# Performance work log

Measured on AMD Instinct MI355X. Metric: run time of the kernel, lower is better.

The kernel has to match this reference:

```python
import jax, jax.numpy as jnp
import numpy as np

L, N, K = 512, 64, 38      # seq_len, batch, input feature size
E, H = 1024, 1024          # embed_size, hidden_size
NUM_LAYERS = 3
C = 38                     # num_classes


def setup_inputs() -> dict:
    key = jax.random.key(0)
    ks = jax.random.split(key, 9)
    s_e = 1.0 / np.sqrt(K)
    s_h = 1.0 / np.sqrt(H)
    return {
        "inputs": jax.random.normal(ks[0], (L, N, K), jnp.float32),
        "emb_W": jax.random.uniform(ks[1], (E, K), jnp.float32, -s_e, s_e),
        "emb_b": jnp.zeros((E,), jnp.float32),
        # GRU weights, PyTorch layout: gates ordered (r, z, n) along 3H axis
        "w_ih": jax.random.uniform(ks[2], (NUM_LAYERS, 3 * H, E), jnp.float32, -s_h, s_h),
        "w_hh": jax.random.uniform(ks[3], (NUM_LAYERS, 3 * H, H), jnp.float32, -s_h, s_h),
        "b_ih": jax.random.uniform(ks[4], (NUM_LAYERS, 3 * H), jnp.float32, -s_h, s_h),
        "b_hh": jax.random.uniform(ks[5], (NUM_LAYERS, 3 * H), jnp.float32, -s_h, s_h),
        "out_W": jax.random.uniform(ks[6], (C, H), jnp.float32, -s_h, s_h),
        "out_b": jnp.zeros((C,), jnp.float32),
    }


def _gru_layer(x, w_ih, w_hh, b_ih, b_hh):
    # x: (L, N, in_dim) -> outputs (L, N, H), final hidden (N, H)
    # Precompute all input projections as one big GEMM: (L, N, 3H)
    xg = jnp.einsum('lni,gi->lng', x, w_ih) + b_ih
    h0 = jnp.zeros((x.shape[1], H), x.dtype)

    def step(h, xg_t):
        hg = h @ w_hh.T + b_hh                      # (N, 3H)
        xr, xz, xn = jnp.split(xg_t, 3, axis=-1)
        hr, hz, hn = jnp.split(hg, 3, axis=-1)
        r = jax.nn.sigmoid(xr + hr)
        z = jax.nn.sigmoid(xz + hz)
        n = jnp.tanh(xn + r * hn)
        h_new = (1.0 - z) * n + z * h
        return h_new, h_new

    h_last, outs = jax.lax.scan(step, h0, xg)
    return outs, h_last


def reference(inputs, emb_W, emb_b, w_ih, w_hh, b_ih, b_hh, out_W, out_b):
    # embedding: Linear(K -> E), applied per timestep
    x = jnp.einsum('lnk,ek->lne', inputs, emb_W) + emb_b  # (L, N, E)
    for l in range(NUM_LAYERS):  # fixed structural loop over layers
        x, _ = _gru_layer(x, w_ih[l], w_hh[l], b_ih[l], b_hh[l])
    # output projection: Linear(H -> C)
    logit = jnp.einsum('lnh,ch->lnc', x, out_W) + out_b    # (L, N, C)
    return logit
```

## Files before the change

kernel.cpp:

```cpp
#include <hip/hip_runtime.h>
#include <hip/hip_fp16.h>
#include <stdint.h>
#include <stddef.h>

typedef _Float16 f16;
typedef _Float16 f16x8 __attribute__((ext_vector_type(8)));
typedef float f32x4 __attribute__((ext_vector_type(4)));

#define SEQL 512
#define NBATCH 64
#define KIN 38
#define KPAD 64
#define EMB 1024
#define HID 1024
#define G3 3072
#define MALL (SEQL*NBATCH)
#define NCLS 38
#define WPAD 1032
#define FS 32


__global__ void k_cvt(const float* __restrict__ s, f16* __restrict__ d, long n) {
  long i = (long)blockIdx.x * blockDim.x + threadIdx.x;
  long stride = (long)gridDim.x * blockDim.x;
  for (; i < n; i += stride) d[i] = (f16)s[i];
}

__global__ void k_zero(int* __restrict__ p, int n) {
  int i = blockIdx.x * 256 + threadIdx.x;
  if (i < n) p[i] = 0;
}

__global__ void k_outw_pad(const float* __restrict__ s, f16* __restrict__ d) {
  int i = blockIdx.x * 256 + threadIdx.x;
  if (i >= 128 * 1024) return;
  int r = i >> 10, c = i & 1023;
  d[i] = (r < NCLS) ? (f16)s[r * 1024 + c] : (f16)0.f;
}

__global__ void k_cvt_in(const float* __restrict__ s, f16* __restrict__ d) {
  int i = blockIdx.x * 256 + threadIdx.x;
  if (i >= MALL * KPAD) return;
  int m = i >> 6, k = i & 63;
  d[i] = (k < KIN) ? (f16)s[m * KIN + k] : (f16)0.f;
}

__global__ void k_prep_w0(const float* __restrict__ wih0, const float* __restrict__ embW,
                          f16* __restrict__ w0) {
  int i = blockIdx.x * 256 + threadIdx.x;
  if (i >= G3 * KPAD) return;
  int g = i >> 6, k = i & 63;
  float sacc = 0.f;
  if (k < KIN) {
    for (int e = 0; e < EMB; ++e) sacc += wih0[g * EMB + e] * embW[e * KIN + k];
  }
  w0[i] = (f16)sacc;
}

__global__ void k_prep_b0(const float* __restrict__ wih0, const float* __restrict__ embB,
                          const float* __restrict__ bih0, float* __restrict__ b0) {
  int g = blockIdx.x * 256 + threadIdx.x;
  if (g >= G3) return;
  float sacc = bih0[g];
  for (int e = 0; e < EMB; ++e) sacc += wih0[g * EMB + e] * embB[e];
  b0[g] = sacc;
}


__global__ __launch_bounds__(256) void k_gemm(
    const f16* __restrict__ A, const f16* __restrict__ B,
    const float* __restrict__ bias,
    f16* __restrict__ C16, float* __restrict__ C32,
    int K, int nvalid, int ldc) {
  __shared__ f16 As[128][40];
  __shared__ f16 Bs[128][40];
  const int tid = threadIdx.x;
  const long brow = (long)blockIdx.x * 128;
  const long bcol = (long)blockIdx.y * 128;
  const int w = tid >> 6, lane = tid & 63;
  const int lr = lane & 15, kg = lane >> 4;
  const int wr = w >> 1, wc = w & 1;

  f32x4 acc[4][4] = {};

  for (int kk = 0; kk < K; kk += 32) {
    __syncthreads();
#pragma unroll
    for (int p = 0; p < 2; ++p) {
      int idx = p * 256 + tid;
      int row = idx >> 2, seg = idx & 3;
      *(float4*)(&As[row][seg * 8]) = *(const float4*)(&A[(brow + row) * K + kk + seg * 8]);
      *(float4*)(&Bs[row][seg * 8]) = *(const float4*)(&B[(bcol + row) * K + kk + seg * 8]);
    }
    __syncthreads();
    f16x8 af[4], bf[4];
#pragma unroll
    for (int i = 0; i < 4; ++i) af[i] = *(const f16x8*)(&As[wr * 64 + i * 16 + lr][kg * 8]);
#pragma unroll
    for (int j = 0; j < 4; ++j) bf[j] = *(const f16x8*)(&Bs[wc * 64 + j * 16 + lr][kg * 8]);
#pragma unroll
    for (int i = 0; i < 4; ++i)
#pragma unroll
      for (int j = 0; j < 4; ++j)
        acc[i][j] = __builtin_amdgcn_mfma_f32_16x16x32_f16(af[i], bf[j], acc[i][j], 0, 0, 0);
  }

#pragma unroll
  for (int j = 0; j < 4; ++j) {
    int col = (int)bcol + wc * 64 + j * 16 + lr;
    float bv = (col < nvalid) ? bias[col] : 0.f;
#pragma unroll
    for (int i = 0; i < 4; ++i) {
#pragma unroll
      for (int r = 0; r < 4; ++r) {
        long row = brow + wr * 64 + i * 16 + kg * 4 + r;
        float v = acc[i][j][r] + bv;
        if (C16) C16[row * ldc + col] = (f16)v;
        else if (col < nvalid) C32[row * ldc + col] = v;
      }
    }
  }
}


__global__ __launch_bounds__(256) void k_rnn(
    f16* __restrict__ xseq,
    f16* __restrict__ hbuf,
    const f16* __restrict__ xg,
    const f16* __restrict__ whhl,
    const float* __restrict__ bhhl,
    int t0, int T, int base,
    int* __restrict__ flags) {
  __shared__ f16 wlds[48 * WPAD];
  const int g = blockIdx.x, j0 = g * 16, tid = threadIdx.x;
  const int w = tid >> 6, lane = tid & 63, lr = lane & 15, kg = lane >> 4;

  for (int idx = tid; idx < 48 * 128; idx += 256) {
    int row = idx >> 7, seg = idx & 127;
    int gt = row >> 4, r = row & 15;
    *(f16x8*)&wlds[row * WPAD + seg * 8] =
        *(const f16x8*)&whhl[(size_t)((gt << 10) + j0 + r) * HID + seg * 8];
  }
  __syncthreads();

  const int j = j0 + lr;
  const float br = bhhl[j], bz = bhhl[1024 + j], bn = bhhl[2048 + j];
  const f16* wr_ = &wlds[(0 * 16 + lr) * WPAD];
  const f16* wz_ = &wlds[(1 * 16 + lr) * WPAD];
  const f16* wn_ = &wlds[(2 * 16 + lr) * WPAD];

  f16 pxr[4], pxz[4], pxn[4];
#pragma unroll
  for (int r = 0; r < 4; ++r) {
    int m = 16 * w + kg * 4 + r;
    pxr[r] = xg[m * G3 + j];
    pxz[r] = xg[m * G3 + 1024 + j];
    pxn[r] = xg[m * G3 + 2048 + j];
  }

  for (int tt = 0; tt < T; ++tt) {
    const int t = t0 + tt;
    f32x4 ar = {}, az = {}, an = {};
    float hp4[4] = {0.f, 0.f, 0.f, 0.f};
    if (t > 0) {
      const int target = base + t;
      int v;
      do {
        v = __hip_atomic_load(&flags[lane * FS], __ATOMIC_ACQUIRE, __HIP_MEMORY_SCOPE_AGENT);
      } while (!__all(v >= target));
      const f16* hb = hbuf + (((t & 1) ^ 1) ? (size_t)(NBATCH * HID) : 0);
      const f16* hbp = hb + g * 1024;
#pragma unroll
      for (int r = 0; r < 4; ++r)
        hp4[r] = (float)hbp[(16 * w + kg * 4 + r) * 16 + lr];
      const f16* hbase = hb + (16 * w + lr) * 16 + (kg & 1) * 8 + (kg >> 1) * 1024;
#pragma unroll 8
      for (int kc = 0; kc < 32; ++kc) {
        f16x8 a = *(const f16x8*)(hbase + kc * 2048);
        int ko = kc * 32 + kg * 8;
        ar = __builtin_amdgcn_mfma_f32_16x16x32_f16(a, *(const f16x8*)(wr_ + ko), ar, 0, 0, 0);
        az = __builtin_amdgcn_mfma_f32_16x16x32_f16(a, *(const f16x8*)(wz_ + ko), az, 0, 0, 0);
        an = __builtin_amdgcn_mfma_f32_16x16x32_f16(a, *(const f16x8*)(wn_ + ko), an, 0, 0, 0);
      }
    }
    f16* hbn = hbuf + ((t & 1) ? (size_t)(NBATCH * HID) : 0) + g * 1024;
    f16* xrow = xseq + (size_t)t * (NBATCH * HID);
#pragma unroll
    for (int r = 0; r < 4; ++r) {
      int m = 16 * w + kg * 4 + r;
      float xr = (float)pxr[r], xz = (float)pxz[r], xn = (float)pxn[r];
      float rr = 1.f / (1.f + __expf(-(xr + ar[r] + br)));
      float zz = 1.f / (1.f + __expf(-(xz + az[r] + bz)));
      float pre = xn + rr * (an[r] + bn);
      float nn = 2.f / (1.f + __expf(-2.f * pre)) - 1.f;
      float hv = (1.f - zz) * nn + zz * hp4[r];
      hbn[m * 16 + lr] = (f16)hv;
      xrow[m * HID + j] = (f16)hv;
    }
    __syncthreads();
    if (tid == 0)
      __hip_atomic_store(&flags[g * FS], base + t + 1, __ATOMIC_RELEASE,
                         __HIP_MEMORY_SCOPE_AGENT);
    if (tt + 1 < T) {
      const f16* xgt = xg + (size_t)(tt + 1) * NBATCH * G3;
#pragma unroll
      for (int r = 0; r < 4; ++r) {
        int m = 16 * w + kg * 4 + r;
        pxr[r] = xgt[m * G3 + j];
        pxz[r] = xgt[m * G3 + 1024 + j];
        pxn[r] = xgt[m * G3 + 2048 + j];
      }
    }
  }
}


extern "C" void kernel_launch(void* const* d_in, const int* in_sizes, int n_in,
                              void* d_out, int out_size, void* d_ws, size_t ws_size,
                              hipStream_t stream) {
  const float* in   = (const float*)d_in[0];
  const float* embW = (const float*)d_in[1];
  const float* embB = (const float*)d_in[2];
  const float* wih  = (const float*)d_in[3];
  const float* whh  = (const float*)d_in[4];
  const float* bih  = (const float*)d_in[5];
  const float* bhh  = (const float*)d_in[6];
  const float* outW = (const float*)d_in[7];
  const float* outB = (const float*)d_in[8];
  float* out = (float*)d_out;

  char* ws = (char*)d_ws;
  size_t off = 0;
  auto alloc = [&](size_t bytes) -> void* {
    void* p = ws + off; off += (bytes + 255) & ~(size_t)255; return p;
  };
  f16* whhL   = (f16*)alloc((size_t)G3 * HID * 2);
  f16* wihL   = (f16*)alloc((size_t)G3 * HID * 2);
  f16* w016   = (f16*)alloc((size_t)G3 * KPAD * 2);
  f16* outw16 = (f16*)alloc(128UL * HID * 2);
  float* b0   = (float*)alloc((size_t)G3 * 4);
  f16* in16   = (f16*)alloc((size_t)MALL * KPAD * 2);
  f16* xseq   = (f16*)alloc((size_t)MALL * HID * 2);
  f16* hbuf   = (f16*)alloc(2UL * NBATCH * HID * 2);
  int* flags  = (int*)alloc(64UL * FS * 4);
  size_t fixed = off;

  int T = 128;
  while (T > 2 && fixed + ((size_t)T * NBATCH * G3 * 2 + 256) > ws_size) T >>= 1;
  f16* xg = (f16*)alloc((size_t)T * NBATCH * G3 * 2);
  if (off > ws_size) return;
  const int NCHUNK = SEQL / T;

  k_zero<<<(64 * FS + 255) / 256, 256, 0, stream>>>(flags, 64 * FS);
  k_outw_pad<<<512, 256, 0, stream>>>(outW, outw16);
  k_cvt_in<<<(MALL * KPAD + 255) / 256, 256, 0, stream>>>(in, in16);
  k_prep_w0<<<(G3 * KPAD + 255) / 256, 256, 0, stream>>>(wih, embW, w016);
  k_prep_b0<<<(G3 + 255) / 256, 256, 0, stream>>>(wih, embB, bih, b0);

  for (int l = 0; l < 3; ++l) {
    k_cvt<<<2048, 256, 0, stream>>>(whh + (size_t)l * G3 * HID, whhL, (long)G3 * HID);
    if (l > 0)
      k_cvt<<<2048, 256, 0, stream>>>(wih + (size_t)l * G3 * EMB, wihL, (long)G3 * HID);

    for (int c = 0; c < NCHUNK; ++c) {
      if (l == 0)
        k_gemm<<<dim3(T * NBATCH / 128, G3 / 128), 256, 0, stream>>>(
            in16 + (size_t)c * T * NBATCH * KPAD, w016, b0, xg, nullptr, KPAD, G3, G3);
      else
        k_gemm<<<dim3(T * NBATCH / 128, G3 / 128), 256, 0, stream>>>(
            xseq + (size_t)c * T * NBATCH * HID, wihL, bih + l * G3, xg, nullptr, HID, G3, G3);
      k_rnn<<<64, 256, 0, stream>>>(xseq, hbuf, xg, whhL, bhh + l * G3,
                                    c * T, T, l * SEQL, flags);
    }
  }
  k_gemm<<<dim3(MALL / 128, 1), 256, 0, stream>>>(xseq, outw16, outB, nullptr, out,
                                                  HID, NCLS, NCLS);
}
```

Baseline: 16.75 ms.

## Transpose gate projections for vector loads and prefetch hidden state in RNN step

The input-projection GEMM now writes its output transposed, so each RNN thread loads its four batch rows per gate with one 4-wide f16 vector load instead of twelve scalar strided loads. In the recurrent step, all 32 hidden-state fragments are loaded into registers before the MFMA chain so global load latency overlaps, and the xseq output store is moved after the flag release to shorten the critical path. Launch bounds are set to one block per SM to allow the larger register footprint. Transposed stores from the GEMM are less coalesced, and the register-heavy prefetch could spill.

```diff
diff --git a/kernel.cpp b/kernel.cpp
--- a/kernel.cpp
+++ b/kernel.cpp
@@ -4,6 +4,7 @@
 #include <stddef.h>
 
 typedef _Float16 f16;
+typedef _Float16 f16x4 __attribute__((ext_vector_type(4)));
 typedef _Float16 f16x8 __attribute__((ext_vector_type(8)));
 typedef float f32x4 __attribute__((ext_vector_type(4)));
 
@@ -70,7 +71,7 @@
 __global__ __launch_bounds__(256) void k_gemm(
     const f16* __restrict__ A, const f16* __restrict__ B,
     const float* __restrict__ bias,
-    f16* __restrict__ C16, float* __restrict__ C32,
+    f16* __restrict__ C16, f16* __restrict__ C16T, float* __restrict__ C32,
     int K, int nvalid, int ldc) {
   __shared__ f16 As[128][40];
   __shared__ f16 Bs[128][40];
@@ -111,25 +112,33 @@
     float bv = (col < nvalid) ? bias[col] : 0.f;
 #pragma unroll
     for (int i = 0; i < 4; ++i) {
-#pragma unroll
-      for (int r = 0; r < 4; ++r) {
-        long row = brow + wr * 64 + i * 16 + kg * 4 + r;
-        float v = acc[i][j][r] + bv;
-        if (C16) C16[row * ldc + col] = (f16)v;
-        else if (col < nvalid) C32[row * ldc + col] = v;
+      if (C16T) {
+        f16x4 pk;
+#pragma unroll
+        for (int r = 0; r < 4; ++r) pk[r] = (f16)(acc[i][j][r] + bv);
+        long row = brow + wr * 64 + i * 16 + kg * 4;
+        *(f16x4*)&C16T[(size_t)col * ldc + row] = pk;
+      } else {
+#pragma unroll
+        for (int r = 0; r < 4; ++r) {
+          long row = brow + wr * 64 + i * 16 + kg * 4 + r;
+          float v = acc[i][j][r] + bv;
+          if (C16) C16[row * ldc + col] = (f16)v;
+          else if (col < nvalid) C32[row * ldc + col] = v;
+        }
       }
     }
   }
 }
 
 
-__global__ __launch_bounds__(256) void k_rnn(
+__global__ __launch_bounds__(256, 1) void k_rnn(
     f16* __restrict__ xseq,
     f16* __restrict__ hbuf,
-    const f16* __restrict__ xg,
+    const f16* __restrict__ xgT,
     const f16* __restrict__ whhl,
     const float* __restrict__ bhhl,
-    int t0, int T, int base,
+    int t0, int T, int LDT, int base,
     int* __restrict__ flags) {
   __shared__ f16 wlds[48 * WPAD];
   const int g = blockIdx.x, j0 = g * 16, tid = threadIdx.x;
@@ -148,15 +157,12 @@
   const f16* wr_ = &wlds[(0 * 16 + lr) * WPAD];
   const f16* wz_ = &wlds[(1 * 16 + lr) * WPAD];
   const f16* wn_ = &wlds[(2 * 16 + lr) * WPAD];
-
-  f16 pxr[4], pxz[4], pxn[4];
-#pragma unroll
-  for (int r = 0; r < 4; ++r) {
-    int m = 16 * w + kg * 4 + r;
-    pxr[r] = xg[m * G3 + j];
-    pxz[r] = xg[m * G3 + 1024 + j];
-    pxn[r] = xg[m * G3 + 2048 + j];
-  }
+  const int mq = 16 * w + kg * 4;
+
+  f16x4 px[3];
+#pragma unroll
+  for (int gt = 0; gt < 3; ++gt)
+    px[gt] = *(const f16x4*)&xgT[(size_t)((gt << 10) + j) * LDT + mq];
 
   for (int tt = 0; tt < T; ++tt) {
     const int t = t0 + tt;
@@ -169,47 +175,55 @@
         v = __hip_atomic_load(&flags[lane * FS], __ATOMIC_ACQUIRE, __HIP_MEMORY_SCOPE_AGENT);
       } while (!__all(v >= target));
       const f16* hb = hbuf + (((t & 1) ^ 1) ? (size_t)(NBATCH * HID) : 0);
+      const f16* hbase = hb + (16 * w + lr) * 16 + (kg & 1) * 8 + (kg >> 1) * 1024;
       const f16* hbp = hb + g * 1024;
-#pragma unroll
-      for (int r = 0; r < 4; ++r)
-        hp4[r] = (float)hbp[(16 * w + kg * 4 + r) * 16 + lr];
-      const f16* hbase = hb + (16 * w + lr) * 16 + (kg & 1) * 8 + (kg >> 1) * 1024;
-#pragma unroll 8
-      for (int kc = 0; kc < 32; ++kc) {
-        f16x8 a = *(const f16x8*)(hbase + kc * 2048);
+      f16x8 fa[16], fb[16];
+#pragma unroll
+      for (int kc = 0; kc < 16; ++kc) fa[kc] = *(const f16x8*)(hbase + kc * 2048);
+#pragma unroll
+      for (int kc = 0; kc < 16; ++kc) fb[kc] = *(const f16x8*)(hbase + (kc + 16) * 2048);
+#pragma unroll
+      for (int r = 0; r < 4; ++r) hp4[r] = (float)hbp[(mq + r) * 16 + lr];
+#pragma unroll
+      for (int kc = 0; kc < 16; ++kc) {
         int ko = kc * 32 + kg * 8;
-        ar = __builtin_amdgcn_mfma_f32_16x16x32_f16(a, *(const f16x8*)(wr_ + ko), ar, 0, 0, 0);
-        az = __builtin_amdgcn_mfma_f32_16x16x32_f16(a, *(const f16x8*)(wz_ + ko), az, 0, 0, 0);
-        an = __builtin_amdgcn_mfma_f32_16x16x32_f16(a, *(const f16x8*)(wn_ + ko), an, 0, 0, 0);
+        ar = __builtin_amdgcn_mfma_f32_16x16x32_f16(fa[kc], *(const f16x8*)(wr_ + ko), ar, 0, 0, 0);
+        az = __builtin_amdgcn_mfma_f32_16x16x32_f16(fa[kc], *(const f16x8*)(wz_ + ko), az, 0, 0, 0);
+        an = __builtin_amdgcn_mfma_f32_16x16x32_f16(fa[kc], *(const f16x8*)(wn_ + ko), an, 0, 0, 0);
       }
+#pragma unroll
+      for (int kc = 0; kc < 16; ++kc) {
+        int ko = (kc + 16) * 32 + kg * 8;
+        ar = __builtin_amdgcn_mfma_f32_16x16x32_f16(fb[kc], *(const f16x8*)(wr_ + ko), ar, 0, 0, 0);
+        az = __builtin_amdgcn_mfma_f32_16x16x32_f16(fb[kc], *(const f16x8*)(wz_ + ko), az, 0, 0, 0);
+        an = __builtin_amdgcn_mfma_f32_16x16x32_f16(fb[kc], *(const f16x8*)(wn_ + ko), an, 0, 0, 0);
+      }
     }
     f16* hbn = hbuf + ((t & 1) ? (size_t)(NBATCH * HID) : 0) + g * 1024;
-    f16* xrow = xseq + (size_t)t * (NBATCH * HID);
+    f16 hv4[4];
 #pragma unroll
     for (int r = 0; r < 4; ++r) {
-      int m = 16 * w + kg * 4 + r;
-      float xr = (float)pxr[r], xz = (float)pxz[r], xn = (float)pxn[r];
+      float xr = (float)px[0][r], xz = (float)px[1][r], xn = (float)px[2][r];
       float rr = 1.f / (1.f + __expf(-(xr + ar[r] + br)));
       float zz = 1.f / (1.f + __expf(-(xz + az[r] + bz)));
       float pre = xn + rr * (an[r] + bn);
       float nn = 2.f / (1.f + __expf(-2.f * pre)) - 1.f;
       float hv = (1.f - zz) * nn + zz * hp4[r];
-      hbn[m * 16 + lr] = (f16)hv;
-      xrow[m * HID + j] = (f16)hv;
+      hv4[r] = (f16)hv;
+      hbn[(mq + r) * 16 + lr] = hv4[r];
     }
     __syncthreads();
     if (tid == 0)
       __hip_atomic_store(&flags[g * FS], base + t + 1, __ATOMIC_RELEASE,
                          __HIP_MEMORY_SCOPE_AGENT);
+    f16* xrow = xseq + (size_t)t * (NBATCH * HID);
+#pragma unroll
+    for (int r = 0; r < 4; ++r) xrow[(mq + r) * HID + j] = hv4[r];
     if (tt + 1 < T) {
-      const f16* xgt = xg + (size_t)(tt + 1) * NBATCH * G3;
-#pragma unroll
-      for (int r = 0; r < 4; ++r) {
-        int m = 16 * w + kg * 4 + r;
-        pxr[r] = xgt[m * G3 + j];
-        pxz[r] = xgt[m * G3 + 1024 + j];
-        pxn[r] = xgt[m * G3 + 2048 + j];
-      }
+      const int mq2 = (tt + 1) * 64 + mq;
+#pragma unroll
+      for (int gt = 0; gt < 3; ++gt)
+        px[gt] = *(const f16x4*)&xgT[(size_t)((gt << 10) + j) * LDT + mq2];
     }
   }
 }
@@ -247,9 +261,10 @@
 
   int T = 128;
   while (T > 2 && fixed + ((size_t)T * NBATCH * G3 * 2 + 256) > ws_size) T >>= 1;
-  f16* xg = (f16*)alloc((size_t)T * NBATCH * G3 * 2);
+  f16* xgT = (f16*)alloc((size_t)T * NBATCH * G3 * 2);
   if (off > ws_size) return;
   const int NCHUNK = SEQL / T;
+  const int LDT = T * NBATCH;
 
   k_zero<<<(64 * FS + 255) / 256, 256, 0, stream>>>(flags, 64 * FS);
   k_outw_pad<<<512, 256, 0, stream>>>(outW, outw16);
@@ -265,14 +280,16 @@
     for (int c = 0; c < NCHUNK; ++c) {
       if (l == 0)
         k_gemm<<<dim3(T * NBATCH / 128, G3 / 128), 256, 0, stream>>>(
-            in16 + (size_t)c * T * NBATCH * KPAD, w016, b0, xg, nullptr, KPAD, G3, G3);
+            in16 + (size_t)c * T * NBATCH * KPAD, w016, b0,
+            nullptr, xgT, nullptr, KPAD, G3, LDT);
       else
         k_gemm<<<dim3(T * NBATCH / 128, G3 / 128), 256, 0, stream>>>(
-            xseq + (size_t)c * T * NBATCH * HID, wihL, bih + l * G3, xg, nullptr, HID, G3, G3);
-      k_rnn<<<64, 256, 0, stream>>>(xseq, hbuf, xg, whhL, bhh + l * G3,
-                                    c * T, T, l * SEQL, flags);
-    }
-  }
-  k_gemm<<<dim3(MALL / 128, 1), 256, 0, stream>>>(xseq, outw16, outB, nullptr, out,
-                                                  HID, NCLS, NCLS);
-}
+            xseq + (size_t)c * T * NBATCH * HID, wihL, bih + l * G3,
+            nullptr, xgT, nullptr, HID, G3, LDT);
+      k_rnn<<<64, 256, 0, stream>>>(xseq, hbuf, xgT, whhL, bhh + l * G3,
+                                    c * T, T, LDT, l * SEQL, flags);
+    }
+  }
+  k_gemm<<<dim3(MALL / 128, 1), 256, 0, stream>>>(xseq, outw16, outB,
+                                                  nullptr, nullptr, out, HID, NCLS, NCLS);
+}
```

Result: slower. 18.31 ms (+9.3%).
